# Kernel tuning notes

Hardware: AMD Instinct MI355X
Metric: run time of the kernel (lower is better)

The kernel has to match this reference:

```python
import jax, jax.numpy as jnp
import numpy as np

B, S, H = 2, 2048, 1024
NH, NKV, HD = 16, 4, 64
G, R = NKV, NH // NKV  # 4 kv groups, 4 query heads per group


def setup_inputs() -> dict:
    key = jax.random.key(0)
    ks = jax.random.split(key, 7)
    scale = 1.0 / np.sqrt(H)
    return {
        "hidden_states": jax.random.normal(ks[0], (B, S, H), jnp.float32),
        "cos": jax.random.normal(ks[1], (S, HD), jnp.float32),
        "sin": jax.random.normal(ks[2], (S, HD), jnp.float32),
        "attention_mask": jnp.ones((B, S), jnp.float32),
        "Wq": jax.random.normal(ks[3], (H, NH * HD), jnp.float32) * scale,
        "Wk": jax.random.normal(ks[4], (H, NKV * HD), jnp.float32) * scale,
        "Wv": jax.random.normal(ks[5], (H, NKV * HD), jnp.float32) * scale,
        "Wo": jax.random.normal(ks[6], (NH * HD, H), jnp.float32) * scale,
    }


def _rotate_half(x):
    h = x.shape[-1] // 2
    return jnp.concatenate([-x[..., h:], x[..., :h]], axis=-1)


def reference(hidden_states, cos, sin, attention_mask, Wq, Wk, Wv, Wo):
    x = hidden_states
    q = (x @ Wq).reshape(B, S, NH, HD)
    k = (x @ Wk).reshape(B, S, NKV, HD)
    v = (x @ Wv).reshape(B, S, NKV, HD)
    # RoPE: cos/sin [S,HD] broadcast over batch and heads
    c = cos[None, :, None, :]
    s = sin[None, :, None, :]
    q = q * c + _rotate_half(q) * s
    k = k * c + _rotate_half(k) * s
    # GQA without materializing repeated KV: q grouped as [B,S,G,R,HD]
    qg = q.reshape(B, S, G, R, HD)
    scores = jnp.einsum("bsgrd,btgd->bgrst", qg, k) / np.sqrt(HD)  # [B,G,R,S,T]
    causal = jnp.tril(jnp.ones((S, S), bool))
    scores = jnp.where(causal[None, None, None], scores, -jnp.inf)
    scores = scores + ((1.0 - attention_mask) * -1e9)[:, None, None, None, :]
    probs = jax.nn.softmax(scores.astype(jnp.float32), axis=-1).astype(q.dtype)
    out = jnp.einsum("bgrst,btgd->bsgrd", probs, v).reshape(B, S, NH * HD)
    return out @ Wo
```

## Files before the change

kernel.cpp:

```cpp
#include <hip/hip_runtime.h>
#include <math.h>

#define B_   2
#define S_   2048
#define H_   1024
#define NH_  16
#define NKV_ 4
#define HD_  64
#define R_   (NH_ / NKV_)
#define QKVW 1536

typedef __attribute__((ext_vector_type(8))) short bf16x8;
typedef __attribute__((ext_vector_type(4))) float f32x4;

__device__ inline short f2bf(float f) {
    unsigned u = __float_as_uint(f);
    u += 0x7FFF + ((u >> 16) & 1);
    return (short)(u >> 16);
}

__device__ inline float exp2fast(float x) {
#if __has_builtin(__builtin_amdgcn_exp2f)
    return __builtin_amdgcn_exp2f(x);
#else
    float r; asm volatile("v_exp_f32 %0, %1\n\ts_nop 1" : "=v"(r) : "v"(x)); return r;
#endif
}

__device__ inline unsigned cvt_pk_bf16(float lo, float hi) {
    unsigned r;
    asm("v_cvt_pk_bf16_f32 %0, %1, %2" : "=v"(r) : "v"(lo), "v"(hi));
    return r;
}

#define LOG2E 1.4426950408889634f

__device__ inline void gload_lds16(const void* gptr, void* lptr) {
    __builtin_amdgcn_global_load_lds(
        (const __attribute__((address_space(1))) unsigned int*)gptr,
        (__attribute__((address_space(3))) unsigned int*)lptr,
        16, 0, 0);
}

__global__ __launch_bounds__(256) void tconv_all(const float* __restrict__ Wq,
                                                 const float* __restrict__ Wk,
                                                 const float* __restrict__ Wv,
                                                 const float* __restrict__ Wo,
                                                 short* __restrict__ Wqkvt,
                                                 short* __restrict__ Wot,
                                                 const float* __restrict__ x,
                                                 short* __restrict__ xb) {
    const int bx = blockIdx.x;
    const int tid = threadIdx.x;

    if (bx >= 640) {
        const size_t e0 = (size_t)(bx - 640) * 16384;
#pragma unroll
        for (int t = 0; t < 8; t++) {
            const size_t i = e0 + ((size_t)t * 256 + tid) * 8;
            float4 a = *(const float4*)&x[i];
            float4 c = *(const float4*)&x[i + 4];
            bf16x8 o;
            o[0] = f2bf(a.x); o[1] = f2bf(a.y); o[2] = f2bf(a.z); o[3] = f2bf(a.w);
            o[4] = f2bf(c.x); o[5] = f2bf(c.y); o[6] = f2bf(c.z); o[7] = f2bf(c.w);
            *(bf16x8*)&xb[i] = o;
        }
        return;
    }

    __shared__ short T[64][68];
    const float* W; short* Wt; int N, idx;
    if (bx < 256)      { W = Wq; Wt = Wqkvt;                     N = 1024; idx = bx; }
    else if (bx < 320) { W = Wk; Wt = Wqkvt + 1024 * 1024;       N = 256;  idx = bx - 256; }
    else if (bx < 384) { W = Wv; Wt = Wqkvt + 1280 * 1024;       N = 256;  idx = bx - 320; }
    else               { W = Wo; Wt = Wot;                       N = 1024; idx = bx - 384; }
    const int ntiles = N >> 6;
    const int n0 = (idx % ntiles) * 64;
    const int k0 = (idx / ntiles) * 64;

    const int r  = tid >> 4;
    const int c4 = (tid & 15) * 4;
#pragma unroll
    for (int t = 0; t < 4; t++) {
        int row = t * 16 + r;
        float4 v = *(const float4*)&W[(size_t)(k0 + row) * N + n0 + c4];
        T[c4 + 0][row] = f2bf(v.x);
        T[c4 + 1][row] = f2bf(v.y);
        T[c4 + 2][row] = f2bf(v.z);
        T[c4 + 3][row] = f2bf(v.w);
    }
    __syncthreads();
#pragma unroll
    for (int t = 0; t < 4; t++) {
        int row = t * 16 + r;
        short4 o = *(short4*)&T[row][c4];
        *(short4*)&Wt[(size_t)(n0 + row) * 1024 + k0 + c4] = o;
    }
}

__global__ __launch_bounds__(256) void gemm1_fused(const short* __restrict__ xb,
                                                   const short* __restrict__ Bt,
                                                   short* __restrict__ qkv,
                                                   short* __restrict__ Vtg,
                                                   const float* __restrict__ cosb,
                                                   const float* __restrict__ sinb) {
    __shared__ short Ah[2][64 * 32];
    __shared__ short Bh[2][128 * 32];

    const int tid  = threadIdx.x;
    const int w    = tid >> 6;
    const int lane = tid & 63;
    const int ln   = lane & 15;
    const int qd   = lane >> 4;
    const int wr   = w >> 1, wc = w & 1;
    const int row0 = blockIdx.y * 64;
    const int col0 = blockIdx.x * 128;

    const int sr = lane >> 2;
    const int sk = (lane & 3) * 8;

    const short* ap = xb + (size_t)(row0 + w * 16 + sr) * 1024 + sk;
    const short* bp0 = Bt + (size_t)(col0 + w * 32 + sr) * 1024 + sk;
    const short* bp1 = Bt + (size_t)(col0 + w * 32 + 16 + sr) * 1024 + sk;

    f32x4 acc[2][4];
#pragma unroll
    for (int mi = 0; mi < 2; mi++)
#pragma unroll
        for (int ni = 0; ni < 4; ni++)
            acc[mi][ni] = (f32x4){0.f, 0.f, 0.f, 0.f};

    gload_lds16(ap,  &Ah[0][(w * 16) * 32]);
    gload_lds16(bp0, &Bh[0][(w * 32) * 32]);
    gload_lds16(bp1, &Bh[0][(w * 32 + 16) * 32]);
    __syncthreads();

    for (int t = 0; t < 32; t++) {
        const int cur = t & 1, nxt = cur ^ 1;
        if (t + 1 < 32) {
            const int k1 = (t + 1) * 32;
            gload_lds16(ap + k1,  &Ah[nxt][(w * 16) * 32]);
            gload_lds16(bp0 + k1, &Bh[nxt][(w * 32) * 32]);
            gload_lds16(bp1 + k1, &Bh[nxt][(w * 32 + 16) * 32]);
        }

        bf16x8 af[2], bfr[4];
#pragma unroll
        for (int mi = 0; mi < 2; mi++)
            af[mi] = *(const bf16x8*)&Ah[cur][(wr * 32 + mi * 16 + ln) * 32 + qd * 8];
#pragma unroll
        for (int ni = 0; ni < 4; ni++)
            bfr[ni] = *(const bf16x8*)&Bh[cur][(wc * 64 + ni * 16 + ln) * 32 + qd * 8];
#pragma unroll
        for (int mi = 0; mi < 2; mi++)
#pragma unroll
            for (int ni = 0; ni < 4; ni++)
                acc[mi][ni] = __builtin_amdgcn_mfma_f32_16x16x32_bf16(af[mi], bfr[ni], acc[mi][ni], 0, 0, 0);

        __syncthreads();
    }

    const int colw = col0 + wc * 64;
    if (colw < H_ + NKV_ * HD_) {
#pragma unroll
        for (int mi = 0; mi < 2; mi++)
#pragma unroll
            for (int i = 0; i < 4; i++) {
                const int row  = row0 + wr * 32 + mi * 16 + qd * 4 + i;
                const int spos = row & (S_ - 1);
                const float* cp = cosb + (size_t)spos * HD_;
                const float* sp = sinb + (size_t)spos * HD_;
                float o0[4];
#pragma unroll
                for (int ni = 0; ni < 2; ni++) {
                    const int d = ni * 16 + ln;
                    float x0 = acc[mi][ni][i], x1 = acc[mi][ni + 2][i];
                    o0[ni]     = x0 * cp[d]      - x1 * sp[d];
                    o0[ni + 2] = x1 * cp[d + 32] + x0 * sp[d + 32];
                }
                short* Cp = qkv + (size_t)row * QKVW + colw + ln;
#pragma unroll
                for (int ni = 0; ni < 4; ni++) Cp[ni * 16] = f2bf(o0[ni]);
            }
    } else {
        const int g = (colw - (H_ + NKV_ * HD_)) >> 6;
#pragma unroll
        for (int mi = 0; mi < 2; mi++) {
            const int rbase = row0 + wr * 32 + mi * 16 + qd * 4;
            const int bg = ((rbase >> 11) * NKV_) + g;
            const int s0 = rbase & (S_ - 1);
#pragma unroll
            for (int ni = 0; ni < 4; ni++) {
                const int d = ni * 16 + ln;
                short4 pk = { f2bf(acc[mi][ni][0]), f2bf(acc[mi][ni][1]),
                              f2bf(acc[mi][ni][2]), f2bf(acc[mi][ni][3]) };
                *(short4*)&Vtg[((size_t)bg * HD_ + d) * S_ + s0] = pk;
            }
        }
    }
}

__global__ __launch_bounds__(256) void gemm2_bt(const short* __restrict__ A, int lda,
                                                const short* __restrict__ Bt,
                                                float* __restrict__ C, int ldc,
                                                int K) {
    __shared__ short Ah[2][64 * 32];
    __shared__ short Bh[2][128 * 32];

    const int tid  = threadIdx.x;
    const int w    = tid >> 6;
    const int lane = tid & 63;
    const int ln   = lane & 15;
    const int qd   = lane >> 4;
    const int wr   = w >> 1, wc = w & 1;
    const int row0 = blockIdx.y * 64;
    const int col0 = blockIdx.x * 128;

    const int sr = lane >> 2;
    const int sk = (lane & 3) * 8;

    const short* ap  = A + (size_t)(row0 + w * 16 + sr) * lda + sk;
    const short* bp0 = Bt + (size_t)(col0 + w * 32 + sr) * K + sk;
    const short* bp1 = Bt + (size_t)(col0 + w * 32 + 16 + sr) * K + sk;

    f32x4 acc[2][4];
#pragma unroll
    for (int mi = 0; mi < 2; mi++)
#pragma unroll
        for (int ni = 0; ni < 4; ni++)
            acc[mi][ni] = (f32x4){0.f, 0.f, 0.f, 0.f};

    const int nt = K >> 5;
    gload_lds16(ap,  &Ah[0][(w * 16) * 32]);
    gload_lds16(bp0, &Bh[0][(w * 32) * 32]);
    gload_lds16(bp1, &Bh[0][(w * 32 + 16) * 32]);
    __syncthreads();

    for (int t = 0; t < nt; t++) {
        const int cur = t & 1, nxt = cur ^ 1;
        if (t + 1 < nt) {
            const int k1 = (t + 1) * 32;
            gload_lds16(ap + k1,  &Ah[nxt][(w * 16) * 32]);
            gload_lds16(bp0 + k1, &Bh[nxt][(w * 32) * 32]);
            gload_lds16(bp1 + k1, &Bh[nxt][(w * 32 + 16) * 32]);
        }

        bf16x8 af[2], bfr[4];
#pragma unroll
        for (int mi = 0; mi < 2; mi++)
            af[mi] = *(const bf16x8*)&Ah[cur][(wr * 32 + mi * 16 + ln) * 32 + qd * 8];
#pragma unroll
        for (int ni = 0; ni < 4; ni++)
            bfr[ni] = *(const bf16x8*)&Bh[cur][(wc * 64 + ni * 16 + ln) * 32 + qd * 8];
#pragma unroll
        for (int mi = 0; mi < 2; mi++)
#pragma unroll
            for (int ni = 0; ni < 4; ni++)
                acc[mi][ni] = __builtin_amdgcn_mfma_f32_16x16x32_bf16(af[mi], bfr[ni], acc[mi][ni], 0, 0, 0);

        __syncthreads();
    }

#pragma unroll
    for (int mi = 0; mi < 2; mi++)
#pragma unroll
        for (int i = 0; i < 4; i++) {
            const size_t row = row0 + wr * 32 + mi * 16 + qd * 4 + i;
            float* Cp = C + row * ldc + col0 + wc * 64 + ln;
#pragma unroll
            for (int ni = 0; ni < 4; ni++) Cp[ni * 16] = acc[mi][ni][i];
        }
}

__global__ __launch_bounds__(512, 2) void attn_kernel(short* __restrict__ qkv,
                                                      const short* __restrict__ Vtg,
                                                      const float* __restrict__ maskb) {
    const int tid  = threadIdx.x;
    const int w    = tid >> 6;
    const int lane = tid & 63;
    const int ln   = lane & 15;
    const int qd   = lane >> 4;

    const int fid = blockIdx.x;
    const int bg  = fid & 7;
    const int u   = fid >> 3;
    const int b   = bg >> 2;
    const int g   = bg & 3;
    const int h   = g * R_ + (u & 3);
    const int a   = u >> 2;

    __shared__ short Ks[2][64 * 72];
    __shared__ short Vt[2][64 * 72];
    __shared__ short Ps[8][16 * 72];
    __shared__ float mskS[2][64];
    short* const ps = Ps[w];

    const short* const Kb = qkv + (size_t)b * S_ * QKVW + H_ + g * HD_;
    const short* const Vb = Vtg + (size_t)bg * HD_ * S_;
    const float* const mb = maskb + b * S_;

    const int fr = tid >> 3;
    const int fc = (tid & 7) * 8;

#pragma unroll 1
    for (int ph = 0; ph < 2; ph++) {
        const int qt   = ph ? (15 - a) : a;
        const int rowb = qt * 128 + w * 16;
        const int ktd  = 2 * qt + (w >> 2);
        const int ntp  = 2 * qt + 2;
        const int qrow = rowb + ln;

        bf16x8 qf0, qf1;
        {
            const short* qp = qkv + (size_t)(b * S_ + rowb + ln) * QKVW + h * HD_;
            qf0 = *(const bf16x8*)&qp[qd * 8];
            qf1 = *(const bf16x8*)&qp[32 + qd * 8];
        }

        f32x4 O[4] = {};
        float mrow = -1e30f, lrow = 0.0f;

        *(bf16x8*)&Ks[0][fr * 72 + fc] = *(const bf16x8*)&Kb[(size_t)fr * QKVW + fc];
        *(bf16x8*)&Vt[0][fr * 72 + fc] = *(const bf16x8*)&Vb[(size_t)fr * S_ + fc];
        if (tid < 64) mskS[0][tid] = (1.0f - mb[tid]) * (-1e9f * LOG2E);
        __syncthreads();

        int cur = 0;
#pragma unroll 1
        for (int kt = 0; kt < ntp; kt++) {
            const int base = kt * 64;
            const bool pf = (kt + 1 < ntp);

            bf16x8 pk, pv;
            float pm = 0.0f;
            if (pf) {
                const int nb = base + 64;
                pk = *(const bf16x8*)&Kb[(size_t)(nb + fr) * QKVW + fc];
                pv = *(const bf16x8*)&Vb[(size_t)fr * S_ + nb + fc];
                if (tid < 64) pm = (1.0f - mb[nb + tid]) * (-1e9f * LOG2E);
            }

            if (kt <= ktd) {
                f32x4 St[4];
#pragma unroll
                for (int kg = 0; kg < 4; kg++) {
                    bf16x8 ka0 = *(const bf16x8*)&Ks[cur][(kg * 16 + ln) * 72 + qd * 8];
                    bf16x8 ka1 = *(const bf16x8*)&Ks[cur][(kg * 16 + ln) * 72 + 32 + qd * 8];
                    f32x4 z = {0.f, 0.f, 0.f, 0.f};
                    z = __builtin_amdgcn_mfma_f32_16x16x32_bf16(ka0, qf0, z, 0, 0, 0);
                    St[kg] = __builtin_amdgcn_mfma_f32_16x16x32_bf16(ka1, qf1, z, 0, 0, 0);
                }

                bf16x8 vb[2][4];
#pragma unroll
                for (int kc2 = 0; kc2 < 2; kc2++)
#pragma unroll
                    for (int dt = 0; dt < 4; dt++)
                        vb[kc2][dt] = *(const bf16x8*)&Vt[cur][(dt * 16 + ln) * 72 + kc2 * 32 + qd * 8];

                float sc[4][4];
#pragma unroll
                for (int kg = 0; kg < 4; kg++) {
                    float4 mv = *(const float4*)&mskS[cur][kg * 16 + qd * 4];
                    sc[kg][0] = fmaf(St[kg][0], 0.125f * LOG2E, mv.x);
                    sc[kg][1] = fmaf(St[kg][1], 0.125f * LOG2E, mv.y);
                    sc[kg][2] = fmaf(St[kg][2], 0.125f * LOG2E, mv.z);
                    sc[kg][3] = fmaf(St[kg][3], 0.125f * LOG2E, mv.w);
                }
                if (kt == ktd) {
#pragma unroll
                    for (int kg = 0; kg < 4; kg++) {
                        const int keyb = base + kg * 16 + qd * 4;
#pragma unroll
                        for (int i = 0; i < 4; i++)
                            if (keyb + i > qrow) sc[kg][i] = -1e30f;
                    }
                }

                float mx = sc[0][0];
#pragma unroll
                for (int kg = 0; kg < 4; kg++)
#pragma unroll
                    for (int i = 0; i < 4; i++) mx = fmaxf(mx, sc[kg][i]);
                mx = fmaxf(mx, __shfl_xor(mx, 16));
                mx = fmaxf(mx, __shfl_xor(mx, 32));

                if (__ballot(mx > mrow + 11.5416f)) {
                    float nm    = fmaxf(mrow, mx);
                    float alpha = exp2fast(mrow - nm);
                    lrow *= alpha;
#pragma unroll
                    for (int i = 0; i < 4; i++) {
                        float av = __shfl(alpha, qd * 4 + i);
#pragma unroll
                        for (int dt = 0; dt < 4; dt++) O[dt][i] *= av;
                    }
                    mrow = nm;
                }
                const float nm = mrow;

                float ls = 0.0f;
#pragma unroll
                for (int kg = 0; kg < 4; kg++)
#pragma unroll
                    for (int i = 0; i < 4; i++) {
                        float p = exp2fast(sc[kg][i] - nm);
                        sc[kg][i] = p;
                        ls += p;
                    }
                ls += __shfl_xor(ls, 16);
                ls += __shfl_xor(ls, 32);
                lrow += ls;

#pragma unroll
                for (int kg = 0; kg < 4; kg++) {
                    uint2 pw;
                    pw.x = cvt_pk_bf16(sc[kg][0], sc[kg][1]);
                    pw.y = cvt_pk_bf16(sc[kg][2], sc[kg][3]);
                    *(uint2*)&ps[ln * 72 + kg * 16 + qd * 4] = pw;
                }

#pragma unroll
                for (int kc2 = 0; kc2 < 2; kc2++) {
                    bf16x8 pa = *(const bf16x8*)&ps[ln * 72 + kc2 * 32 + qd * 8];
#pragma unroll
                    for (int dt = 0; dt < 4; dt++)
                        O[dt] = __builtin_amdgcn_mfma_f32_16x16x32_bf16(pa, vb[kc2][dt], O[dt], 0, 0, 0);
                }
            }

            if (pf) {
                const int nxt = cur ^ 1;
                *(bf16x8*)&Ks[nxt][fr * 72 + fc] = pk;
                *(bf16x8*)&Vt[nxt][fr * 72 + fc] = pv;
                if (tid < 64) mskS[nxt][tid] = pm;
            }
            __syncthreads();
            cur ^= 1;
        }

#pragma unroll
        for (int i = 0; i < 4; i++) {
            float li  = __shfl(lrow, qd * 4 + i);
            float inv = 1.0f / li;
            const int row = rowb + qd * 4 + i;
            short* op = qkv + (size_t)(b * S_ + row) * QKVW + h * HD_ + ln;
#pragma unroll
            for (int dt = 0; dt < 4; dt++) op[dt * 16] = f2bf(O[dt][i] * inv);
        }
    }
}

extern "C" void kernel_launch(void* const* d_in, const int* in_sizes, int n_in,
                              void* d_out, int out_size, void* d_ws, size_t ws_size,
                              hipStream_t stream) {
    const float* x     = (const float*)d_in[0];
    const float* cosb  = (const float*)d_in[1];
    const float* sinb  = (const float*)d_in[2];
    const float* maskb = (const float*)d_in[3];
    const float* Wq    = (const float*)d_in[4];
    const float* Wk    = (const float*)d_in[5];
    const float* Wv    = (const float*)d_in[6];
    const float* Wo    = (const float*)d_in[7];

    const int M = B_ * S_;

    short* qkv   = (short*)d_ws;
    short* Wqkvt = qkv + (size_t)M * QKVW;
    short* Wot   = Wqkvt + (size_t)QKVW * H_;
    short* Vtg   = Wot + (size_t)H_ * H_;
    short* xb    = (short*)d_out;
    float* out   = (float*)d_out;

    dim3 blk(256);

    tconv_all<<<dim3(896), blk, 0, stream>>>(Wq, Wk, Wv, Wo, Wqkvt, Wot, x, xb);

    gemm1_fused<<<dim3(QKVW / 128, M / 64), blk, 0, stream>>>(xb, Wqkvt, qkv, Vtg, cosb, sinb);

    attn_kernel<<<dim3(256), dim3(512), 0, stream>>>(qkv, Vtg, maskb);

    gemm2_bt<<<dim3(H_ / 128, M / 64), blk, 0, stream>>>(qkv, QKVW, Wot, out, H_, H_);
}
```

Measured before the change: 183.7 us.

## Fuse x bf16 conversion into GEMM1 and restructure attention to 256-thread blocks

Removes the separate fp32-to-bf16 conversion of hidden states from the weight-transpose kernel and instead loads fp32 x directly in gemm1, converting it in registers before storing to LDS. This drops one global round-trip of x but replaces async global-to-LDS loads with synchronous register loads. The attention kernel changes from 512-thread blocks that each process two query tiles in sequence to 256-thread blocks with 512 blocks, where each wave handles 32 query rows (two row groups) so K/V fragments are reused across both. It also adds s_setprio around the MFMA sections.

```diff
diff --git a/kernel.cpp b/kernel.cpp
--- a/kernel.cpp
+++ b/kernel.cpp
@@ -47,28 +47,10 @@
                                                  const float* __restrict__ Wv,
                                                  const float* __restrict__ Wo,
                                                  short* __restrict__ Wqkvt,
-                                                 short* __restrict__ Wot,
-                                                 const float* __restrict__ x,
-                                                 short* __restrict__ xb) {
+                                                 short* __restrict__ Wot) {
+    __shared__ short T[64][68];
     const int bx = blockIdx.x;
     const int tid = threadIdx.x;
-
-    if (bx >= 640) {
-        const size_t e0 = (size_t)(bx - 640) * 16384;
-#pragma unroll
-        for (int t = 0; t < 8; t++) {
-            const size_t i = e0 + ((size_t)t * 256 + tid) * 8;
-            float4 a = *(const float4*)&x[i];
-            float4 c = *(const float4*)&x[i + 4];
-            bf16x8 o;
-            o[0] = f2bf(a.x); o[1] = f2bf(a.y); o[2] = f2bf(a.z); o[3] = f2bf(a.w);
-            o[4] = f2bf(c.x); o[5] = f2bf(c.y); o[6] = f2bf(c.z); o[7] = f2bf(c.w);
-            *(bf16x8*)&xb[i] = o;
-        }
-        return;
-    }
-
-    __shared__ short T[64][68];
     const float* W; short* Wt; int N, idx;
     if (bx < 256)      { W = Wq; Wt = Wqkvt;                     N = 1024; idx = bx; }
     else if (bx < 320) { W = Wk; Wt = Wqkvt + 1024 * 1024;       N = 256;  idx = bx - 256; }
@@ -98,7 +80,7 @@
     }
 }
 
-__global__ __launch_bounds__(256) void gemm1_fused(const short* __restrict__ xb,
+__global__ __launch_bounds__(256) void gemm1_fused(const float* __restrict__ x,
                                                    const short* __restrict__ Bt,
                                                    short* __restrict__ qkv,
                                                    short* __restrict__ Vtg,
@@ -118,8 +100,10 @@
 
     const int sr = lane >> 2;
     const int sk = (lane & 3) * 8;
-
-    const short* ap = xb + (size_t)(row0 + w * 16 + sr) * 1024 + sk;
+    const int ar  = tid >> 2;
+    const int ac8 = (tid & 3) * 8;
+
+    const float* xp  = x + (size_t)(row0 + ar) * 1024 + ac8;
     const short* bp0 = Bt + (size_t)(col0 + w * 32 + sr) * 1024 + sk;
     const short* bp1 = Bt + (size_t)(col0 + w * 32 + 16 + sr) * 1024 + sk;
 
@@ -130,7 +114,14 @@
         for (int ni = 0; ni < 4; ni++)
             acc[mi][ni] = (f32x4){0.f, 0.f, 0.f, 0.f};
 
-    gload_lds16(ap,  &Ah[0][(w * 16) * 32]);
+    {
+        float4 a1 = *(const float4*)xp;
+        float4 a2 = *(const float4*)(xp + 4);
+        bf16x8 o;
+        o[0]=f2bf(a1.x); o[1]=f2bf(a1.y); o[2]=f2bf(a1.z); o[3]=f2bf(a1.w);
+        o[4]=f2bf(a2.x); o[5]=f2bf(a2.y); o[6]=f2bf(a2.z); o[7]=f2bf(a2.w);
+        *(bf16x8*)&Ah[0][ar * 32 + ac8] = o;
+    }
     gload_lds16(bp0, &Bh[0][(w * 32) * 32]);
     gload_lds16(bp1, &Bh[0][(w * 32 + 16) * 32]);
     __syncthreads();
@@ -139,9 +130,14 @@
         const int cur = t & 1, nxt = cur ^ 1;
         if (t + 1 < 32) {
             const int k1 = (t + 1) * 32;
-            gload_lds16(ap + k1,  &Ah[nxt][(w * 16) * 32]);
             gload_lds16(bp0 + k1, &Bh[nxt][(w * 32) * 32]);
             gload_lds16(bp1 + k1, &Bh[nxt][(w * 32 + 16) * 32]);
+            float4 a1 = *(const float4*)(xp + k1);
+            float4 a2 = *(const float4*)(xp + k1 + 4);
+            bf16x8 o;
+            o[0]=f2bf(a1.x); o[1]=f2bf(a1.y); o[2]=f2bf(a1.z); o[3]=f2bf(a1.w);
+            o[4]=f2bf(a2.x); o[5]=f2bf(a2.y); o[6]=f2bf(a2.z); o[7]=f2bf(a2.w);
+            *(bf16x8*)&Ah[nxt][ar * 32 + ac8] = o;
         }
 
         bf16x8 af[2], bfr[4];
@@ -272,26 +268,29 @@
         }
 }
 
-__global__ __launch_bounds__(512, 2) void attn_kernel(short* __restrict__ qkv,
-                                                      const short* __restrict__ Vtg,
-                                                      const float* __restrict__ maskb) {
+__global__ __launch_bounds__(256) void attn_kernel(short* __restrict__ qkv,
+                                                   const short* __restrict__ Vtg,
+                                                   const float* __restrict__ maskb) {
     const int tid  = threadIdx.x;
     const int w    = tid >> 6;
     const int lane = tid & 63;
     const int ln   = lane & 15;
     const int qd   = lane >> 4;
 
-    const int fid = blockIdx.x;
-    const int bg  = fid & 7;
-    const int u   = fid >> 3;
+    const int i   = blockIdx.x;
+    const int bg  = i & 7;
+    const int u   = i >> 3;
     const int b   = bg >> 2;
     const int g   = bg & 3;
-    const int h   = g * R_ + (u & 3);
-    const int a   = u >> 2;
+    const int hr  = u & 3;
+    const int t   = (u >> 2) & 7;
+    const int slot = u >> 5;
+    const int h   = g * R_ + hr;
+    const int qt  = slot ? (15 - t) : t;
 
     __shared__ short Ks[2][64 * 72];
     __shared__ short Vt[2][64 * 72];
-    __shared__ short Ps[8][16 * 72];
+    __shared__ short Ps[4][16 * 72];
     __shared__ float mskS[2][64];
     short* const ps = Ps[w];
 
@@ -299,118 +298,128 @@
     const short* const Vb = Vtg + (size_t)bg * HD_ * S_;
     const float* const mb = maskb + b * S_;
 
-    const int fr = tid >> 3;
-    const int fc = (tid & 7) * 8;
-
+    const int fr = tid >> 2;
+    const int fc = (tid & 3) * 16;
+
+    const int rowb = qt * 128 + w * 32;
+    const int ktd  = 2 * qt + (w >> 1);
+    const int nt   = 2 * qt + 2;
+
+    bf16x8 qf[2][2];
+#pragma unroll
+    for (int rg = 0; rg < 2; rg++) {
+        const short* qp = qkv + (size_t)(b * S_ + rowb + rg * 16 + ln) * QKVW + h * HD_;
+        qf[rg][0] = *(const bf16x8*)&qp[qd * 8];
+        qf[rg][1] = *(const bf16x8*)&qp[32 + qd * 8];
+    }
+
+    f32x4 O[2][4] = {};
+    float mrow[2] = {-1e30f, -1e30f};
+    float lrow[2] = {0.0f, 0.0f};
+
+    *(bf16x8*)&Ks[0][fr * 72 + fc]     = *(const bf16x8*)&Kb[(size_t)fr * QKVW + fc];
+    *(bf16x8*)&Ks[0][fr * 72 + fc + 8] = *(const bf16x8*)&Kb[(size_t)fr * QKVW + fc + 8];
+    *(bf16x8*)&Vt[0][fr * 72 + fc]     = *(const bf16x8*)&Vb[(size_t)fr * S_ + fc];
+    *(bf16x8*)&Vt[0][fr * 72 + fc + 8] = *(const bf16x8*)&Vb[(size_t)fr * S_ + fc + 8];
+    if (tid < 64) mskS[0][tid] = (1.0f - mb[tid]) * (-1e9f * LOG2E);
+    __syncthreads();
+
+    int cur = 0;
 #pragma unroll 1
-    for (int ph = 0; ph < 2; ph++) {
-        const int qt   = ph ? (15 - a) : a;
-        const int rowb = qt * 128 + w * 16;
-        const int ktd  = 2 * qt + (w >> 2);
-        const int ntp  = 2 * qt + 2;
-        const int qrow = rowb + ln;
-
-        bf16x8 qf0, qf1;
-        {
-            const short* qp = qkv + (size_t)(b * S_ + rowb + ln) * QKVW + h * HD_;
-            qf0 = *(const bf16x8*)&qp[qd * 8];
-            qf1 = *(const bf16x8*)&qp[32 + qd * 8];
-        }
-
-        f32x4 O[4] = {};
-        float mrow = -1e30f, lrow = 0.0f;
-
-        *(bf16x8*)&Ks[0][fr * 72 + fc] = *(const bf16x8*)&Kb[(size_t)fr * QKVW + fc];
-        *(bf16x8*)&Vt[0][fr * 72 + fc] = *(const bf16x8*)&Vb[(size_t)fr * S_ + fc];
-        if (tid < 64) mskS[0][tid] = (1.0f - mb[tid]) * (-1e9f * LOG2E);
-        __syncthreads();
-
-        int cur = 0;
-#pragma unroll 1
-        for (int kt = 0; kt < ntp; kt++) {
-            const int base = kt * 64;
-            const bool pf = (kt + 1 < ntp);
-
-            bf16x8 pk, pv;
-            float pm = 0.0f;
-            if (pf) {
-                const int nb = base + 64;
-                pk = *(const bf16x8*)&Kb[(size_t)(nb + fr) * QKVW + fc];
-                pv = *(const bf16x8*)&Vb[(size_t)fr * S_ + nb + fc];
-                if (tid < 64) pm = (1.0f - mb[nb + tid]) * (-1e9f * LOG2E);
+    for (int kt = 0; kt < nt; kt++) {
+        const int base = kt * 64;
+        const bool pf = (kt + 1 < nt);
+
+        bf16x8 pk0, pk1, pv0, pv1;
+        float pm = 0.0f;
+        if (pf) {
+            const int nb = base + 64;
+            pk0 = *(const bf16x8*)&Kb[(size_t)(nb + fr) * QKVW + fc];
+            pk1 = *(const bf16x8*)&Kb[(size_t)(nb + fr) * QKVW + fc + 8];
+            pv0 = *(const bf16x8*)&Vb[(size_t)fr * S_ + nb + fc];
+            pv1 = *(const bf16x8*)&Vb[(size_t)fr * S_ + nb + fc + 8];
+            if (tid < 64) pm = (1.0f - mb[nb + tid]) * (-1e9f * LOG2E);
+        }
+
+        if (kt <= ktd) {
+            f32x4 St[2][4];
+            __builtin_amdgcn_s_setprio(1);
+#pragma unroll
+            for (int kg = 0; kg < 4; kg++) {
+                bf16x8 ka0 = *(const bf16x8*)&Ks[cur][(kg * 16 + ln) * 72 + qd * 8];
+                bf16x8 ka1 = *(const bf16x8*)&Ks[cur][(kg * 16 + ln) * 72 + 32 + qd * 8];
+#pragma unroll
+                for (int rg = 0; rg < 2; rg++) {
+                    f32x4 z = {0.f, 0.f, 0.f, 0.f};
+                    z = __builtin_amdgcn_mfma_f32_16x16x32_bf16(ka0, qf[rg][0], z, 0, 0, 0);
+                    St[rg][kg] = __builtin_amdgcn_mfma_f32_16x16x32_bf16(ka1, qf[rg][1], z, 0, 0, 0);
+                }
             }
-
-            if (kt <= ktd) {
-                f32x4 St[4];
+            __builtin_amdgcn_s_setprio(0);
+
+            bf16x8 vb[2][4];
+#pragma unroll
+            for (int kc2 = 0; kc2 < 2; kc2++)
+#pragma unroll
+                for (int dt = 0; dt < 4; dt++)
+                    vb[kc2][dt] = *(const bf16x8*)&Vt[cur][(dt * 16 + ln) * 72 + kc2 * 32 + qd * 8];
+
+            float mt[4][4];
+#pragma unroll
+            for (int kg = 0; kg < 4; kg++) {
+                float4 mv = *(const float4*)&mskS[cur][kg * 16 + qd * 4];
+                mt[kg][0] = mv.x; mt[kg][1] = mv.y; mt[kg][2] = mv.z; mt[kg][3] = mv.w;
+            }
+
+            const bool diag = (kt == ktd);
+
+#pragma unroll
+            for (int rg = 0; rg < 2; rg++) {
+                const int qrow = rowb + rg * 16 + ln;
+                float sc[4][4];
 #pragma unroll
                 for (int kg = 0; kg < 4; kg++) {
-                    bf16x8 ka0 = *(const bf16x8*)&Ks[cur][(kg * 16 + ln) * 72 + qd * 8];
-                    bf16x8 ka1 = *(const bf16x8*)&Ks[cur][(kg * 16 + ln) * 72 + 32 + qd * 8];
-                    f32x4 z = {0.f, 0.f, 0.f, 0.f};
-                    z = __builtin_amdgcn_mfma_f32_16x16x32_bf16(ka0, qf0, z, 0, 0, 0);
-                    St[kg] = __builtin_amdgcn_mfma_f32_16x16x32_bf16(ka1, qf1, z, 0, 0, 0);
-                }
-
-                bf16x8 vb[2][4];
-#pragma unroll
-                for (int kc2 = 0; kc2 < 2; kc2++)
-#pragma unroll
-                    for (int dt = 0; dt < 4; dt++)
-                        vb[kc2][dt] = *(const bf16x8*)&Vt[cur][(dt * 16 + ln) * 72 + kc2 * 32 + qd * 8];
-
-                float sc[4][4];
-#pragma unroll
-                for (int kg = 0; kg < 4; kg++) {
-                    float4 mv = *(const float4*)&mskS[cur][kg * 16 + qd * 4];
-                    sc[kg][0] = fmaf(St[kg][0], 0.125f * LOG2E, mv.x);
-                    sc[kg][1] = fmaf(St[kg][1], 0.125f * LOG2E, mv.y);
-                    sc[kg][2] = fmaf(St[kg][2], 0.125f * LOG2E, mv.z);
-                    sc[kg][3] = fmaf(St[kg][3], 0.125f * LOG2E, mv.w);
-                }
-                if (kt == ktd) {
-#pragma unroll
-                    for (int kg = 0; kg < 4; kg++) {
-                        const int keyb = base + kg * 16 + qd * 4;
-#pragma unroll
-                        for (int i = 0; i < 4; i++)
-                            if (keyb + i > qrow) sc[kg][i] = -1e30f;
+                    const int keyb = base + kg * 16 + qd * 4;
+#pragma unroll
+                    for (int i2 = 0; i2 < 4; i2++) {
+                        float v = fmaf(St[rg][kg][i2], 0.125f * LOG2E, mt[kg][i2]);
+                        sc[kg][i2] = (diag && (keyb + i2 > qrow)) ? -1e30f : v;
                     }
                 }
-
                 float mx = sc[0][0];
 #pragma unroll
                 for (int kg = 0; kg < 4; kg++)
 #pragma unroll
-                    for (int i = 0; i < 4; i++) mx = fmaxf(mx, sc[kg][i]);
+                    for (int i2 = 0; i2 < 4; i2++) mx = fmaxf(mx, sc[kg][i2]);
                 mx = fmaxf(mx, __shfl_xor(mx, 16));
                 mx = fmaxf(mx, __shfl_xor(mx, 32));
 
-                if (__ballot(mx > mrow + 11.5416f)) {
-                    float nm    = fmaxf(mrow, mx);
-                    float alpha = exp2fast(mrow - nm);
-                    lrow *= alpha;
-#pragma unroll
-                    for (int i = 0; i < 4; i++) {
-                        float av = __shfl(alpha, qd * 4 + i);
-#pragma unroll
-                        for (int dt = 0; dt < 4; dt++) O[dt][i] *= av;
+                if (__ballot(mx > mrow[rg] + 11.5416f)) {
+                    float nm    = fmaxf(mrow[rg], mx);
+                    float alpha = exp2fast(mrow[rg] - nm);
+                    lrow[rg] *= alpha;
+#pragma unroll
+                    for (int i2 = 0; i2 < 4; i2++) {
+                        float av = __shfl(alpha, qd * 4 + i2);
+#pragma unroll
+                        for (int dt = 0; dt < 4; dt++) O[rg][dt][i2] *= av;
                     }
-                    mrow = nm;
-                }
-                const float nm = mrow;
+                    mrow[rg] = nm;
+                }
+                const float nm = mrow[rg];
 
                 float ls = 0.0f;
 #pragma unroll
                 for (int kg = 0; kg < 4; kg++)
 #pragma unroll
-                    for (int i = 0; i < 4; i++) {
-                        float p = exp2fast(sc[kg][i] - nm);
-                        sc[kg][i] = p;
+                    for (int i2 = 0; i2 < 4; i2++) {
+                        float p = exp2fast(sc[kg][i2] - nm);
+                        sc[kg][i2] = p;
                         ls += p;
                     }
                 ls += __shfl_xor(ls, 16);
                 ls += __shfl_xor(ls, 32);
-                lrow += ls;
+                lrow[rg] += ls;
 
 #pragma unroll
                 for (int kg = 0; kg < 4; kg++) {
@@ -420,35 +429,41 @@
                     *(uint2*)&ps[ln * 72 + kg * 16 + qd * 4] = pw;
                 }
 
+                __builtin_amdgcn_s_setprio(1);
 #pragma unroll
                 for (int kc2 = 0; kc2 < 2; kc2++) {
                     bf16x8 pa = *(const bf16x8*)&ps[ln * 72 + kc2 * 32 + qd * 8];
 #pragma unroll
                     for (int dt = 0; dt < 4; dt++)
-                        O[dt] = __builtin_amdgcn_mfma_f32_16x16x32_bf16(pa, vb[kc2][dt], O[dt], 0, 0, 0);
-                }
+                        O[rg][dt] = __builtin_amdgcn_mfma_f32_16x16x32_bf16(pa, vb[kc2][dt], O[rg][dt], 0, 0, 0);
+                }
+                __builtin_amdgcn_s_setprio(0);
             }
-
-            if (pf) {
-                const int nxt = cur ^ 1;
-                *(bf16x8*)&Ks[nxt][fr * 72 + fc] = pk;
-                *(bf16x8*)&Vt[nxt][fr * 72 + fc] = pv;
-                if (tid < 64) mskS[nxt][tid] = pm;
-            }
-            __syncthreads();
-            cur ^= 1;
-        }
-
-#pragma unroll
-        for (int i = 0; i < 4; i++) {
-            float li  = __shfl(lrow, qd * 4 + i);
+        }
+
+        if (pf) {
+            const int nxt = cur ^ 1;
+            *(bf16x8*)&Ks[nxt][fr * 72 + fc]     = pk0;
+            *(bf16x8*)&Ks[nxt][fr * 72 + fc + 8] = pk1;
+            *(bf16x8*)&Vt[nxt][fr * 72 + fc]     = pv0;
+            *(bf16x8*)&Vt[nxt][fr * 72 + fc + 8] = pv1;
+            if (tid < 64) mskS[nxt][tid] = pm;
+        }
+        __syncthreads();
+        cur ^= 1;
+    }
+
+#pragma unroll
+    for (int rg = 0; rg < 2; rg++)
+#pragma unroll
+        for (int i2 = 0; i2 < 4; i2++) {
+            float li  = __shfl(lrow[rg], qd * 4 + i2);
             float inv = 1.0f / li;
-            const int row = rowb + qd * 4 + i;
+            const int row = rowb + rg * 16 + qd * 4 + i2;
             short* op = qkv + (size_t)(b * S_ + row) * QKVW + h * HD_ + ln;
 #pragma unroll
-            for (int dt = 0; dt < 4; dt++) op[dt * 16] = f2bf(O[dt][i] * inv);
-        }
-    }
+            for (int dt = 0; dt < 4; dt++) op[dt * 16] = f2bf(O[rg][dt][i2] * inv);
+        }
 }
 
 extern "C" void kernel_launch(void* const* d_in, const int* in_sizes, int n_in,
@@ -469,16 +484,15 @@
     short* Wqkvt = qkv + (size_t)M * QKVW;
     short* Wot   = Wqkvt + (size_t)QKVW * H_;
     short* Vtg   = Wot + (size_t)H_ * H_;
-    short* xb    = (short*)d_out;
     float* out   = (float*)d_out;
 
     dim3 blk(256);
 
-    tconv_all<<<dim3(896), blk, 0, stream>>>(Wq, Wk, Wv, Wo, Wqkvt, Wot, x, xb);
-
-    gemm1_fused<<<dim3(QKVW / 128, M / 64), blk, 0, stream>>>(xb, Wqkvt, qkv, Vtg, cosb, sinb);
-
-    attn_kernel<<<dim3(256), dim3(512), 0, stream>>>(qkv, Vtg, maskb);
+    tconv_all<<<dim3(640), blk, 0, stream>>>(Wq, Wk, Wv, Wo, Wqkvt, Wot);
+
+    gemm1_fused<<<dim3(QKVW / 128, M / 64), blk, 0, stream>>>(x, Wqkvt, qkv, Vtg, cosb, sinb);
+
+    attn_kernel<<<dim3(512), blk, 0, stream>>>(qkv, Vtg, maskb);
 
     gemm2_bt<<<dim3(H_ / 128, M / 64), blk, 0, stream>>>(qkv, QKVW, Wot, out, H_, H_);
 }
```

After: 206.8 us. 12.6% more time.
